# Performance work log

Measured on AMD Instinct MI355X. Metric: run time of the kernel, lower is better.

Reference implementation:

```python
import jax, jax.numpy as jnp
import numpy as np

N_NODES = 100000
N_EDGES = 1600000
N_UNARY = 16
N_BINARY = 4
# Each clause: (literal column indices, signs); sign=-1 means negated literal.
# KENN t-conorm boost: delta = w * sign * softmax(sign * preactivation over clause literals)
UNARY_CLAUSES = [([0, 1], [-1.0, 1.0]),
                 ([2, 3], [-1.0, 1.0]),
                 ([4, 5, 6], [-1.0, 1.0, 1.0]),
                 ([7, 8], [1.0, -1.0])]
# Joined matrix columns: [0:16]=1.P*, [16:32]=2.P*, [32:36]=R*
BINARY_CLAUSES = [([0, 32, 16], [-1.0, -1.0, 1.0]),   # n1.P0, nR0, 2.P0
                  ([1, 33, 17], [-1.0, -1.0, 1.0]),   # n1.P1, nR1, 2.P1
                  ([34, 35], [-1.0, 1.0]),            # nR2, R3
                  ([2, 18], [-1.0, 1.0])]             # n1.P2, 2.P2


def _knowledge_enhancer(x, clauses, weights):
    """Sum of per-clause deltas scattered back into full predicate space."""
    delta = jnp.zeros_like(x)
    for ci, (idx, signs) in enumerate(clauses):
        idx = np.asarray(idx)
        s = jnp.asarray(signs, dtype=x.dtype)
        sel = x[:, idx] * s                                  # [n, L] signed literal preactivations
        d = s * jax.nn.softmax(sel, axis=1) * weights[ci]    # [n, L]
        delta = delta.at[:, idx].add(d)
    return delta


def setup_inputs() -> dict:
    key = jax.random.key(0)
    k1, k2, k3, k4 = jax.random.split(key, 4)
    return {
        "unary": jax.random.normal(k1, (N_NODES, N_UNARY), jnp.float32),
        "binary": jax.random.normal(k2, (N_EDGES, N_BINARY), jnp.float32),
        "index1": jax.random.randint(k3, (N_EDGES,), 0, N_NODES),
        "index2": jax.random.randint(k4, (N_EDGES,), 0, N_NODES),
        "unary_cw": jnp.full((len(UNARY_CLAUSES),), 0.5, jnp.float32),
        "binary_cw": jnp.full((len(BINARY_CLAUSES),), 0.5, jnp.float32),
    }


def reference(unary, binary, index1, index2, unary_cw, binary_cw):
    # unary KnowledgeEnhancer
    u = unary + _knowledge_enhancer(unary, UNARY_CLAUSES, unary_cw)
    # Join: gather unary features for both endpoints of each edge
    joined = jnp.concatenate([u[index1], u[index2], binary], axis=1)  # [m, 2U+B]
    # binary KnowledgeEnhancer over joined matrix
    db = _knowledge_enhancer(joined, BINARY_CLAUSES, binary_cw)
    # GroupBy: scatter-reduce unary parts back to nodes
    delta_up = (jax.ops.segment_sum(db[:, :N_UNARY], index1, num_segments=N_NODES)
                + jax.ops.segment_sum(db[:, N_UNARY:2 * N_UNARY], index2, num_segments=N_NODES))
    delta_bp = db[:, 2 * N_UNARY:]
    # activation is identity (default)
    return u + delta_up, binary + delta_bp
```

## Files before the change

kernel.cpp:

```cpp
#include <hip/hip_runtime.h>
#include <math.h>

#define N_NODES 100000
#define N_EDGES 1600000
#define N_UNARY 16

#define NCHUNK 16
#define CH 6250
#define EPW 512
#define NWG_E 3125
#define CAP 112
#define NSLICE 16
#define PER_SLICE 196

#define FPSCALE 8192.0f
#define INV_FPSCALE (1.0f / 8192.0f)

typedef unsigned long long u64;

__device__ inline long long pack3(float a, float b, float c) {
    long long qa = (long long)__float2int_rn(a * FPSCALE);
    long long qb = (long long)__float2int_rn(b * FPSCALE);
    long long qc = (long long)__float2int_rn(c * FPSCALE);
    return (qa << 42) + (qb << 21) + qc;
}

__device__ inline u64 enc_rec(int local, float a, float b, float c) {
    int qa = __float2int_rn(a * FPSCALE);
    int qb = __float2int_rn(b * FPSCALE);
    int qc = __float2int_rn(c * FPSCALE);
    return ((u64)local << 42) |
           ((u64)((unsigned)qa & 0x3FFFu) << 28) |
           ((u64)((unsigned)qb & 0x3FFFu) << 14) |
           ((u64)((unsigned)qc & 0x3FFFu));
}

__device__ inline unsigned f2bf(float f) {
    union { float f; unsigned u; } v; v.f = f;
    return ((v.u + 0x7FFFu + ((v.u >> 16) & 1u)) >> 16) & 0xFFFFu;
}
__device__ inline float bf2f(unsigned h) {
    union { unsigned u; float f; } v; v.u = h << 16; return v.f;
}

__device__ inline void stage_rec(int node, float d0, float d1, float d2,
                                 unsigned int* __restrict__ cnt,
                                 u64* __restrict__ stg,
                                 u64* __restrict__ spill)
{
    int c = node / CH;
    int local = node - c * CH;
    unsigned slot = atomicAdd(&cnt[c], 1u);
    if (slot < CAP)
        stg[c * CAP + slot] = enc_rec(local, d0, d1, d2);
    else
        atomicAdd(&spill[node], (u64)pack3(d0, d1, d2));
}

__global__ __launch_bounds__(256) void kenn_node_kernel(
    const float* __restrict__ unary,
    const float* __restrict__ ucw,
    float* __restrict__ out_nodes,
    float4* __restrict__ u3tab,
    u64* __restrict__ u3bf,
    u64* __restrict__ acc)
{
    int n = blockIdx.x * blockDim.x + threadIdx.x;
    if (n >= N_NODES) return;

    acc[n] = 0ull;

    const float w0 = ucw[0], w1 = ucw[1], w2 = ucw[2], w3 = ucw[3];

    const float4* row = reinterpret_cast<const float4*>(unary + (size_t)n * N_UNARY);
    float4 r0 = row[0], r1 = row[1], r2 = row[2], r3 = row[3];

    float x0 = r0.x, x1 = r0.y, x2 = r0.z, x3 = r0.w;
    float x4 = r1.x, x5 = r1.y, x6 = r1.z, x7 = r1.w;
    float x8 = r2.x;

    {
        float t = __expf(-x0 - x1);
        float p1 = 1.0f / (1.0f + t);
        float p0 = 1.0f - p1;
        x0 = r0.x - w0 * p0;
        x1 = r0.y + w0 * p1;
    }
    {
        float t = __expf(-x2 - x3);
        float p1 = 1.0f / (1.0f + t);
        float p0 = 1.0f - p1;
        x2 = r0.z - w1 * p0;
        x3 = r0.w + w1 * p1;
    }
    {
        float s0 = -x4, s1 = x5, s2 = x6;
        float m = fmaxf(fmaxf(s0, s1), s2);
        float e0 = __expf(s0 - m), e1 = __expf(s1 - m), e2 = __expf(s2 - m);
        float inv = 1.0f / (e0 + e1 + e2);
        x4 = r1.x - w2 * e0 * inv;
        x5 = r1.y + w2 * e1 * inv;
        x6 = r1.z + w2 * e2 * inv;
    }
    {
        float t = __expf(-x8 - x7);
        float p0 = 1.0f / (1.0f + t);
        float p1 = 1.0f - p0;
        x7 = r1.w + w3 * p0;
        x8 = r2.x - w3 * p1;
    }

    float4* orow = reinterpret_cast<float4*>(out_nodes + (size_t)n * N_UNARY);
    orow[0] = make_float4(x0, x1, x2, x3);
    orow[1] = make_float4(x4, x5, x6, x7);
    orow[2] = make_float4(x8, r2.y, r2.z, r2.w);
    orow[3] = r3;

    u3tab[n] = make_float4(x0, x1, x2, x3);
    u3bf[n] = (u64)f2bf(x0) | ((u64)f2bf(x1) << 16)
            | ((u64)f2bf(x2) << 32) | ((u64)f2bf(x3) << 48);
}

__device__ inline void edge_math(float ax, float ay, float az,
                                 float bx, float by, float bz, float4 bin,
                                 float w0, float w1, float w2, float w3,
                                 float4& bout,
                                 float& d1c0, float& d1c1, float& d1c2,
                                 float& d2c0, float& d2c1, float& d2c2)
{
    float dbin0, dbin1, dbin2, dbin3;
    {
        float s0 = -ax, s1 = -bin.x, s2 = bx;
        float m = fmaxf(fmaxf(s0, s1), s2);
        float e0 = __expf(s0 - m), e1 = __expf(s1 - m), e2 = __expf(s2 - m);
        float inv = 1.0f / (e0 + e1 + e2);
        d1c0  = -w0 * e0 * inv;
        dbin0 = -w0 * e1 * inv;
        d2c0  =  w0 * e2 * inv;
    }
    {
        float s0 = -ay, s1 = -bin.y, s2 = by;
        float m = fmaxf(fmaxf(s0, s1), s2);
        float e0 = __expf(s0 - m), e1 = __expf(s1 - m), e2 = __expf(s2 - m);
        float inv = 1.0f / (e0 + e1 + e2);
        d1c1  = -w1 * e0 * inv;
        dbin1 = -w1 * e1 * inv;
        d2c1  =  w1 * e2 * inv;
    }
    {
        float t = __expf(-bin.z - bin.w);
        float p1 = 1.0f / (1.0f + t);
        float p0 = 1.0f - p1;
        dbin2 = -w2 * p0;
        dbin3 =  w2 * p1;
    }
    {
        float t = __expf(-az - bz);
        float p1 = 1.0f / (1.0f + t);
        float p0 = 1.0f - p1;
        d1c2 = -w3 * p0;
        d2c2 =  w3 * p1;
    }
    bout = make_float4(bin.x + dbin0, bin.y + dbin1, bin.z + dbin2, bin.w + dbin3);
}

__device__ inline void gather_u3(const u64* __restrict__ u3bf, int i,
                                 float& x, float& y, float& z)
{
    u64 g = __hip_atomic_load(&u3bf[i], __ATOMIC_RELAXED, __HIP_MEMORY_SCOPE_AGENT);
    x = bf2f((unsigned)(g & 0xFFFFu));
    y = bf2f((unsigned)((g >> 16) & 0xFFFFu));
    z = bf2f((unsigned)((g >> 32) & 0xFFFFu));
}

__global__ __launch_bounds__(256) void kenn_edge_bin_kernel(
    const float* __restrict__ binary,
    const int* __restrict__ idx1,
    const int* __restrict__ idx2,
    const float* __restrict__ bcw,
    const u64* __restrict__ u3bf,
    u64* __restrict__ rec,
    unsigned int* __restrict__ counts,
    u64* __restrict__ spill,
    float* __restrict__ out_binary)
{
    __shared__ unsigned int cnt[NCHUNK];
    __shared__ u64 stg[NCHUNK * CAP];

    if (threadIdx.x < NCHUNK) cnt[threadIdx.x] = 0;
    __syncthreads();

    const float w0 = bcw[0], w1 = bcw[1], w2 = bcw[2], w3 = bcw[3];

    const int e0 = blockIdx.x * EPW + threadIdx.x;
    const int e1 = e0 + 256;

    int i1a = idx1[e0], i2a = idx2[e0];
    int i1b = idx1[e1], i2b = idx2[e1];
    float4 bina = reinterpret_cast<const float4*>(binary)[e0];
    float4 binb = reinterpret_cast<const float4*>(binary)[e1];

    float aax, aay, aaz, bax, bay, baz;
    float abx, aby, abz, bbx, bby, bbz;
    gather_u3(u3bf, i1a, aax, aay, aaz);
    gather_u3(u3bf, i2a, bax, bay, baz);
    gather_u3(u3bf, i1b, abx, aby, abz);
    gather_u3(u3bf, i2b, bbx, bby, bbz);

    float4 bouta, boutb;
    float a1c0, a1c1, a1c2, a2c0, a2c1, a2c2;
    float b1c0, b1c1, b1c2, b2c0, b2c1, b2c2;
    edge_math(aax, aay, aaz, bax, bay, baz, bina, w0, w1, w2, w3,
              bouta, a1c0, a1c1, a1c2, a2c0, a2c1, a2c2);
    edge_math(abx, aby, abz, bbx, bby, bbz, binb, w0, w1, w2, w3,
              boutb, b1c0, b1c1, b1c2, b2c0, b2c1, b2c2);

    reinterpret_cast<float4*>(out_binary)[e0] = bouta;
    reinterpret_cast<float4*>(out_binary)[e1] = boutb;

    stage_rec(i1a, a1c0, a1c1, a1c2, cnt, stg, spill);
    stage_rec(i2a, a2c0, a2c1, a2c2, cnt, stg, spill);
    stage_rec(i1b, b1c0, b1c1, b1c2, cnt, stg, spill);
    stage_rec(i2b, b2c0, b2c1, b2c2, cnt, stg, spill);
    __syncthreads();

    const size_t wg = blockIdx.x;
    const int wv = threadIdx.x >> 6;
    const int ln = threadIdx.x & 63;
#pragma unroll
    for (int j = 0; j < 4; ++j) {
        int c = wv * 4 + j;
        unsigned n = min(cnt[c], (unsigned)CAP);
        for (unsigned i = ln; i < n; i += 64)
            rec[((wg * NCHUNK + c) * CAP) + i] = stg[c * CAP + i];
    }
    if (threadIdx.x < NCHUNK)
        counts[wg * NCHUNK + threadIdx.x] = min(cnt[threadIdx.x], (unsigned)CAP);
}

__global__ __launch_bounds__(1024) void kenn_accum_kernel(
    const u64* __restrict__ rec,
    const unsigned int* __restrict__ counts,
    u64* __restrict__ partial)
{
    extern __shared__ u64 accL[];
    __shared__ unsigned int cnts[PER_SLICE];

    const int wg = blockIdx.x;
    const int c = wg >> 4;
    const int s = wg & (NSLICE - 1);
    const int pbase = s * PER_SLICE;
    const int pend = min(pbase + PER_SLICE, NWG_E);
    const int np = pend - pbase;

    for (int j = threadIdx.x; j < np; j += blockDim.x)
        cnts[j] = counts[(size_t)(pbase + j) * NCHUNK + c];
    for (int i = threadIdx.x; i < CH; i += blockDim.x)
        accL[i] = 0ull;
    __syncthreads();

    const int wave = threadIdx.x >> 6;
    const int lane = threadIdx.x & 63;
    for (int j = wave; j < np; j += 16) {
        const int cnt = (int)cnts[j];
        const u64* rp = rec + ((size_t)(pbase + j) * NCHUNK + c) * CAP;
        for (int i = lane; i < cnt; i += 64) {
            u64 r = rp[i];
            int local = (int)(r >> 42);
            long long q0 = ((long long)(r << 22)) >> 50;
            long long q1 = ((long long)(r << 36)) >> 50;
            long long q2 = ((long long)(r << 50)) >> 50;
            u64 pkt = (u64)((q0 << 42) + (q1 << 21) + q2);
            atomicAdd(&accL[local], pkt);
        }
    }
    __syncthreads();

    u64* pout = partial + (size_t)wg * CH;
    for (int i = threadIdx.x; i < CH; i += blockDim.x)
        pout[i] = accL[i];
}

__global__ __launch_bounds__(256) void kenn_final_kernel(
    const u64* __restrict__ partial,
    const u64* __restrict__ spill,
    const float4* __restrict__ u3tab,
    float* __restrict__ out_nodes)
{
    int n = blockIdx.x * blockDim.x + threadIdx.x;
    if (n >= N_NODES) return;

    int c = n / CH;
    int local = n - c * CH;
    const u64* pp = partial + (size_t)(c * NSLICE) * CH + local;

    long long t = (long long)spill[n];
#pragma unroll
    for (int s = 0; s < NSLICE; ++s)
        t += (long long)pp[(size_t)s * CH];

    long long qc = (t << 43) >> 43;
    t = (t - qc) >> 21;
    long long qb = (t << 43) >> 43;
    long long qa = (t - qb) >> 21;

    float4 u = u3tab[n];
    reinterpret_cast<float4*>(out_nodes + (size_t)n * N_UNARY)[0] =
        make_float4(u.x + (float)qa * INV_FPSCALE,
                    u.y + (float)qb * INV_FPSCALE,
                    u.z + (float)qc * INV_FPSCALE,
                    u.w);
}

__global__ __launch_bounds__(256) void kenn_edge_atomic_kernel(
    const float* __restrict__ binary,
    const int* __restrict__ idx1,
    const int* __restrict__ idx2,
    const float* __restrict__ bcw,
    const float4* __restrict__ u3tab,
    u64* __restrict__ acc,
    float* __restrict__ out_binary)
{
    int e = blockIdx.x * blockDim.x + threadIdx.x;
    if (e >= N_EDGES) return;

    const float w0 = bcw[0], w1 = bcw[1], w2 = bcw[2], w3 = bcw[3];

    int i1 = idx1[e];
    int i2 = idx2[e];
    float4 bin = reinterpret_cast<const float4*>(binary)[e];
    float4 a = u3tab[i1];
    float4 b = u3tab[i2];

    float4 bout;
    float d1c0, d1c1, d1c2, d2c0, d2c1, d2c2;
    edge_math(a.x, a.y, a.z, b.x, b.y, b.z, bin, w0, w1, w2, w3,
              bout, d1c0, d1c1, d1c2, d2c0, d2c1, d2c2);

    reinterpret_cast<float4*>(out_binary)[e] = bout;

    atomicAdd(&acc[i1], (u64)pack3(d1c0, d1c1, d1c2));
    atomicAdd(&acc[i2], (u64)pack3(d2c0, d2c1, d2c2));
}

__global__ __launch_bounds__(256) void kenn_fixup_kernel(
    const u64* __restrict__ acc,
    const float4* __restrict__ u3tab,
    float* __restrict__ out_nodes)
{
    int n = blockIdx.x * blockDim.x + threadIdx.x;
    if (n >= N_NODES) return;

    long long t = (long long)acc[n];
    long long qc = (t << 43) >> 43;
    t = (t - qc) >> 21;
    long long qb = (t << 43) >> 43;
    long long qa = (t - qb) >> 21;

    float4 u = u3tab[n];
    reinterpret_cast<float4*>(out_nodes + (size_t)n * N_UNARY)[0] =
        make_float4(u.x + (float)qa * INV_FPSCALE,
                    u.y + (float)qb * INV_FPSCALE,
                    u.z + (float)qc * INV_FPSCALE,
                    u.w);
}

extern "C" void kernel_launch(void* const* d_in, const int* in_sizes, int n_in,
                              void* d_out, int out_size, void* d_ws, size_t ws_size,
                              hipStream_t stream) {
    const float* unary    = (const float*)d_in[0];
    const float* binary   = (const float*)d_in[1];
    const int*   index1   = (const int*)d_in[2];
    const int*   index2   = (const int*)d_in[3];
    const float* unary_cw = (const float*)d_in[4];
    const float* bin_cw   = (const float*)d_in[5];

    float* out_nodes  = (float*)d_out;
    float* out_binary = (float*)d_out + (size_t)N_NODES * N_UNARY;

    char* base = (char*)d_ws;
    size_t off_u3   = 0;
    size_t off_bf   = off_u3 + (size_t)N_NODES * 16;
    size_t off_acc  = off_bf + (size_t)N_NODES * 8;
    size_t off_rec  = off_acc + (size_t)N_NODES * 8;
    size_t off_cnt  = off_rec + (size_t)NWG_E * NCHUNK * CAP * 8;
    size_t off_par  = (off_cnt + (size_t)NWG_E * NCHUNK * 4 + 255) & ~(size_t)255;
    size_t need     = off_par + (size_t)NCHUNK * NSLICE * CH * 8;

    float4* u3tab = (float4*)(base + off_u3);
    u64* u3bf = (u64*)(base + off_bf);
    u64* acc = (u64*)(base + off_acc);

    dim3 blockN(256), gridN((N_NODES + 255) / 256);

    kenn_node_kernel<<<gridN, blockN, 0, stream>>>(unary, unary_cw, out_nodes,
                                                   u3tab, u3bf, acc);

    if (ws_size >= need) {
        u64* rec = (u64*)(base + off_rec);
        unsigned int* counts = (unsigned int*)(base + off_cnt);
        u64* partials = (u64*)(base + off_par);

        kenn_edge_bin_kernel<<<dim3(NWG_E), dim3(256), 0, stream>>>(
            binary, index1, index2, bin_cw, u3bf, rec, counts, acc, out_binary);

        kenn_accum_kernel<<<dim3(NCHUNK * NSLICE), dim3(1024), CH * 8, stream>>>(
            rec, counts, partials);

        kenn_final_kernel<<<gridN, blockN, 0, stream>>>(partials, acc, u3tab,
                                                        out_nodes);
    } else {
        kenn_edge_atomic_kernel<<<dim3((N_EDGES + 255) / 256), dim3(256), 0, stream>>>(
            binary, index1, index2, bin_cw, u3tab, acc, out_binary);
        kenn_fixup_kernel<<<gridN, blockN, 0, stream>>>(acc, u3tab, out_nodes);
    }
}
```

Before: 52.16 us.

## Stage edge records per wave instead of per workgroup to drop barriers

Each wave in the edge kernel now keeps its own LDS staging buckets and counters, and becomes its own producer with a smaller per-chunk capacity. The two workgroup barriers are replaced by wave-local lgkmcnt waits, and the accumulate kernel reads four times as many producer segments. The unary gather also switches from a relaxed atomic load to a plain load. In exchange, the record and count buffers get larger, the accumulate kernel walks more and shorter segments, and overflow past the smaller per-wave capacity sends more records to the global spill atomics.

Measured after the change: 66.83 us. 1.28x slower.

```diff
diff --git a/kernel.cpp b/kernel.cpp
--- a/kernel.cpp
+++ b/kernel.cpp
@@ -9,9 +9,11 @@
 #define CH 6250
 #define EPW 512
 #define NWG_E 3125
-#define CAP 112
+#define NWAVES 4
+#define NPROD (NWG_E * NWAVES)
+#define CAP_W 36
 #define NSLICE 16
-#define PER_SLICE 196
+#define PER_SLICE 782
 
 #define FPSCALE 8192.0f
 #define INV_FPSCALE (1.0f / 8192.0f)
@@ -44,15 +46,15 @@
 }
 
 __device__ inline void stage_rec(int node, float d0, float d1, float d2,
-                                 unsigned int* __restrict__ cnt,
-                                 u64* __restrict__ stg,
+                                 unsigned int* __restrict__ wcnt,
+                                 u64* __restrict__ wstg,
                                  u64* __restrict__ spill)
 {
     int c = node / CH;
     int local = node - c * CH;
-    unsigned slot = atomicAdd(&cnt[c], 1u);
-    if (slot < CAP)
-        stg[c * CAP + slot] = enc_rec(local, d0, d1, d2);
+    unsigned slot = atomicAdd(&wcnt[c], 1u);
+    if (slot < CAP_W)
+        wstg[c * CAP_W + slot] = enc_rec(local, d0, d1, d2);
     else
         atomicAdd(&spill[node], (u64)pack3(d0, d1, d2));
 }
@@ -167,7 +169,7 @@
 __device__ inline void gather_u3(const u64* __restrict__ u3bf, int i,
                                  float& x, float& y, float& z)
 {
-    u64 g = __hip_atomic_load(&u3bf[i], __ATOMIC_RELAXED, __HIP_MEMORY_SCOPE_AGENT);
+    u64 g = u3bf[i];
     x = bf2f((unsigned)(g & 0xFFFFu));
     y = bf2f((unsigned)((g >> 16) & 0xFFFFu));
     z = bf2f((unsigned)((g >> 32) & 0xFFFFu));
@@ -184,11 +186,16 @@
     u64* __restrict__ spill,
     float* __restrict__ out_binary)
 {
-    __shared__ unsigned int cnt[NCHUNK];
-    __shared__ u64 stg[NCHUNK * CAP];
-
-    if (threadIdx.x < NCHUNK) cnt[threadIdx.x] = 0;
-    __syncthreads();
+    __shared__ unsigned int cnt[NWAVES * NCHUNK];
+    __shared__ u64 stg[NWAVES * NCHUNK * CAP_W];
+
+    const int wv = threadIdx.x >> 6;
+    const int ln = threadIdx.x & 63;
+    unsigned int* wcnt = cnt + wv * NCHUNK;
+    u64* wstg = stg + wv * NCHUNK * CAP_W;
+
+    if (ln < NCHUNK) wcnt[ln] = 0;
+    asm volatile("s_waitcnt lgkmcnt(0)" ::: "memory");
 
     const float w0 = bcw[0], w1 = bcw[1], w2 = bcw[2], w3 = bcw[3];
 
@@ -218,24 +225,21 @@
     reinterpret_cast<float4*>(out_binary)[e0] = bouta;
     reinterpret_cast<float4*>(out_binary)[e1] = boutb;
 
-    stage_rec(i1a, a1c0, a1c1, a1c2, cnt, stg, spill);
-    stage_rec(i2a, a2c0, a2c1, a2c2, cnt, stg, spill);
-    stage_rec(i1b, b1c0, b1c1, b1c2, cnt, stg, spill);
-    stage_rec(i2b, b2c0, b2c1, b2c2, cnt, stg, spill);
-    __syncthreads();
-
-    const size_t wg = blockIdx.x;
-    const int wv = threadIdx.x >> 6;
-    const int ln = threadIdx.x & 63;
+    stage_rec(i1a, a1c0, a1c1, a1c2, wcnt, wstg, spill);
+    stage_rec(i2a, a2c0, a2c1, a2c2, wcnt, wstg, spill);
+    stage_rec(i1b, b1c0, b1c1, b1c2, wcnt, wstg, spill);
+    stage_rec(i2b, b2c0, b2c1, b2c2, wcnt, wstg, spill);
+    asm volatile("s_waitcnt lgkmcnt(0)" ::: "memory");
+
+    const size_t prod = (size_t)blockIdx.x * NWAVES + wv;
 #pragma unroll
-    for (int j = 0; j < 4; ++j) {
-        int c = wv * 4 + j;
-        unsigned n = min(cnt[c], (unsigned)CAP);
+    for (int c = 0; c < NCHUNK; ++c) {
+        unsigned n = min(wcnt[c], (unsigned)CAP_W);
         for (unsigned i = ln; i < n; i += 64)
-            rec[((wg * NCHUNK + c) * CAP) + i] = stg[c * CAP + i];
-    }
-    if (threadIdx.x < NCHUNK)
-        counts[wg * NCHUNK + threadIdx.x] = min(cnt[threadIdx.x], (unsigned)CAP);
+            rec[(prod * NCHUNK + c) * CAP_W + i] = wstg[c * CAP_W + i];
+    }
+    if (ln < NCHUNK)
+        counts[prod * NCHUNK + ln] = min(wcnt[ln], (unsigned)CAP_W);
 }
 
 __global__ __launch_bounds__(1024) void kenn_accum_kernel(
@@ -250,7 +254,7 @@
     const int c = wg >> 4;
     const int s = wg & (NSLICE - 1);
     const int pbase = s * PER_SLICE;
-    const int pend = min(pbase + PER_SLICE, NWG_E);
+    const int pend = min(pbase + PER_SLICE, NPROD);
     const int np = pend - pbase;
 
     for (int j = threadIdx.x; j < np; j += blockDim.x)
@@ -263,7 +267,7 @@
     const int lane = threadIdx.x & 63;
     for (int j = wave; j < np; j += 16) {
         const int cnt = (int)cnts[j];
-        const u64* rp = rec + ((size_t)(pbase + j) * NCHUNK + c) * CAP;
+        const u64* rp = rec + ((size_t)(pbase + j) * NCHUNK + c) * CAP_W;
         for (int i = lane; i < cnt; i += 64) {
             u64 r = rp[i];
             int local = (int)(r >> 42);
@@ -383,8 +387,8 @@
     size_t off_bf   = off_u3 + (size_t)N_NODES * 16;
     size_t off_acc  = off_bf + (size_t)N_NODES * 8;
     size_t off_rec  = off_acc + (size_t)N_NODES * 8;
-    size_t off_cnt  = off_rec + (size_t)NWG_E * NCHUNK * CAP * 8;
-    size_t off_par  = (off_cnt + (size_t)NWG_E * NCHUNK * 4 + 255) & ~(size_t)255;
+    size_t off_cnt  = off_rec + (size_t)NPROD * NCHUNK * CAP_W * 8;
+    size_t off_par  = (off_cnt + (size_t)NPROD * NCHUNK * 4 + 255) & ~(size_t)255;
     size_t need     = off_par + (size_t)NCHUNK * NSLICE * CH * 8;
 
     float4* u3tab = (float4*)(base + off_u3);
```
